# Kernel optimization log

Hardware: AMD Instinct MI355X
Metric: run time of the kernel (lower is better)

## Reference

```python
import jax, jax.numpy as jnp
import numpy as np

DIM = 1024
HEADS = 16
HDIM = DIM // HEADS
MLP_HID = 4096
LN_EPS = 1e-5
NORM_EPS = 1e-12  # F.normalize eps


def _layernorm(x, g, b):
    mu = jnp.mean(x, axis=-1, keepdims=True)
    var = jnp.mean(jnp.square(x - mu), axis=-1, keepdims=True)
    return (x - mu) / jnp.sqrt(var + LN_EPS) * g + b


def _l2norm(x):
    n = jnp.linalg.norm(x, axis=-1, keepdims=True)
    return x / jnp.maximum(n, NORM_EPS)


def setup_inputs() -> dict:
    key = jax.random.key(0)
    ks = jax.random.split(key, 8)
    s = 0.02
    x = jax.random.normal(ks[0], (2, 2048, DIM), dtype=jnp.float32)
    w_qkv = jax.random.normal(ks[1], (3 * DIM, DIM), dtype=jnp.float32) * s  # torch Linear weight (out,in)
    w_proj = jax.random.normal(ks[2], (DIM, DIM), dtype=jnp.float32) * s
    temp = jnp.ones((HEADS, 1, 1), dtype=jnp.float32)
    w1 = jax.random.normal(ks[3], (MLP_HID, DIM), dtype=jnp.float32) * s
    b1 = jnp.zeros((MLP_HID,), dtype=jnp.float32)
    w2 = jax.random.normal(ks[4], (DIM, MLP_HID), dtype=jnp.float32) * s
    b2 = jnp.zeros((DIM,), dtype=jnp.float32)
    ln1_g = jnp.ones((DIM,), dtype=jnp.float32)
    ln1_b = jnp.zeros((DIM,), dtype=jnp.float32)
    ln2_g = jnp.ones((DIM,), dtype=jnp.float32)
    ln2_b = jnp.zeros((DIM,), dtype=jnp.float32)
    return {"x": x, "ln1_g": ln1_g, "ln1_b": ln1_b, "w_qkv": w_qkv,
            "w_proj": w_proj, "temp": temp, "ln2_g": ln2_g, "ln2_b": ln2_b,
            "w1": w1, "b1": b1, "w2": w2, "b2": b2}


def reference(x, ln1_g, ln1_b, w_qkv, w_proj, temp, ln2_g, ln2_b, w1, b1, w2, b2):
    b, n, c = x.shape
    # --- MHSA with L2-normalized q,k and learnable per-head temperature ---
    h = _layernorm(x, ln1_g, ln1_b)
    qkv = h @ w_qkv.T                             # [b,n,3c]
    qkv = qkv.reshape(b, n, 3, HEADS, HDIM).transpose(2, 0, 3, 1, 4)  # [3,b,h,n,d]
    q, k, v = qkv[0], qkv[1], qkv[2]
    q = _l2norm(q)
    k = _l2norm(k)
    attn = jnp.einsum('bhnd,bhmd->bhnm', q, k) * temp  # temp [h,1,1] broadcasts
    attn = jax.nn.softmax(attn, axis=-1)
    out = jnp.einsum('bhnm,bhmd->bhnd', attn, v)       # [b,h,n,d]
    out = out.transpose(0, 2, 1, 3).reshape(b, n, c)
    x = x + out @ w_proj.T
    # --- MLP ---
    h = _layernorm(x, ln2_g, ln2_b)
    h = jax.nn.gelu(h @ w1.T + b1, approximate=False)
    x = x + h @ w2.T + b2
    return x
```

## Files before the change

kernel.cpp:

```cpp
#include <hip/hip_runtime.h>
#include <cstdint>
#include <cstddef>

typedef unsigned short u16;
typedef __attribute__((ext_vector_type(8))) short short8;
typedef __attribute__((ext_vector_type(4))) float f32x4;
typedef __attribute__((ext_vector_type(4))) float float4v;
typedef __attribute__((ext_vector_type(4))) u16 u16x4;

__device__ __forceinline__ u16 f2bf(float f) {
  union { float f; uint32_t u; } v; v.f = f;
  uint32_t u = v.u;
  return (u16)((u + 0x7FFFu + ((u >> 16) & 1u)) >> 16);
}
__device__ __forceinline__ float bf2f(u16 s) {
  union { uint32_t u; float f; } v; v.u = ((uint32_t)s) << 16; return v.f;
}

__device__ __forceinline__ float fast_exp2(float x) {
#if __has_builtin(__builtin_amdgcn_exp2f)
  return __builtin_amdgcn_exp2f(x);
#else
  return exp2f(x);
#endif
}

__device__ __forceinline__ void gload16(const u16* g, u16* l) {
  __builtin_amdgcn_global_load_lds((const __attribute__((address_space(1))) void*)g,
                                   (__attribute__((address_space(3))) void*)l,
                                   16, 0, 0);
}

__global__ __launch_bounds__(256) void k_cvt(const float* __restrict__ in, u16* __restrict__ out, int n4) {
  int i = blockIdx.x * 256 + threadIdx.x;
  if (i >= n4) return;
  float4v v = *(const float4v*)(in + (size_t)i * 4);
  u16x4 o;
  #pragma unroll
  for (int j = 0; j < 4; j++) o[j] = f2bf(v[j]);
  *(u16x4*)(out + (size_t)i * 4) = o;
}

__global__ __launch_bounds__(256) void k_ln(const float* __restrict__ x, const float* __restrict__ g,
                                            const float* __restrict__ b, u16* __restrict__ out) {
  int row = blockIdx.x, tid = threadIdx.x;
  int wid = tid >> 6;
  const float* xr = x + (size_t)row * 1024;
  float4v v = *(const float4v*)(xr + tid * 4);
  float s = v[0] + v[1] + v[2] + v[3];
  float sq = v[0]*v[0] + v[1]*v[1] + v[2]*v[2] + v[3]*v[3];
  #pragma unroll
  for (int m = 1; m <= 32; m <<= 1) { s += __shfl_xor(s, m); sq += __shfl_xor(sq, m); }
  __shared__ float ss[4], ssq[4];
  if ((tid & 63) == 0) { ss[wid] = s; ssq[wid] = sq; }
  __syncthreads();
  s = ss[0] + ss[1] + ss[2] + ss[3];
  sq = ssq[0] + ssq[1] + ssq[2] + ssq[3];
  float mu = s * (1.0f/1024.0f);
  float var = sq * (1.0f/1024.0f) - mu*mu;
  float rs = rsqrtf(var + 1e-5f);
  u16x4 o;
  #pragma unroll
  for (int j = 0; j < 4; j++) {
    float y = (v[j] - mu) * rs * g[tid*4+j] + b[tid*4+j];
    o[j] = f2bf(y);
  }
  *(u16x4*)(out + (size_t)row * 1024 + tid * 4) = o;
}

__global__ __launch_bounds__(256) void k_redln(const float* __restrict__ x, const u16* __restrict__ P,
                                               const float* __restrict__ g, const float* __restrict__ b,
                                               float* __restrict__ x1, u16* __restrict__ h2) {
  int row = blockIdx.x, tid = threadIdx.x;
  int wid = tid >> 6;
  size_t off = (size_t)row * 1024 + tid * 4;
  float4v v = *(const float4v*)(x + off);
  #pragma unroll
  for (int z = 0; z < 4; z++) {
    u16x4 p = *(const u16x4*)(P + (size_t)z * 4194304 + off);
    #pragma unroll
    for (int j = 0; j < 4; j++) v[j] += bf2f(p[j]);
  }
  *(float4v*)(x1 + off) = v;
  float s = v[0] + v[1] + v[2] + v[3];
  float sq = v[0]*v[0] + v[1]*v[1] + v[2]*v[2] + v[3]*v[3];
  #pragma unroll
  for (int m = 1; m <= 32; m <<= 1) { s += __shfl_xor(s, m); sq += __shfl_xor(sq, m); }
  __shared__ float ss[4], ssq[4];
  if ((tid & 63) == 0) { ss[wid] = s; ssq[wid] = sq; }
  __syncthreads();
  s = ss[0] + ss[1] + ss[2] + ss[3];
  sq = ssq[0] + ssq[1] + ssq[2] + ssq[3];
  float mu = s * (1.0f/1024.0f);
  float var = sq * (1.0f/1024.0f) - mu*mu;
  float rs = rsqrtf(var + 1e-5f);
  u16x4 o;
  #pragma unroll
  for (int j = 0; j < 4; j++) o[j] = f2bf((v[j] - mu) * rs * g[tid*4+j] + b[tid*4+j]);
  *(u16x4*)(h2 + off) = o;
}

template<int EPI>
__global__ __launch_bounds__(512, 2) void k_g256(const u16* __restrict__ A, const u16* __restrict__ B,
                                                 const float* __restrict__ bias, u16* __restrict__ Cb,
                                                 int M, int N, int K, int Ksub) {
  extern __shared__ __align__(16) u16 smem[];
  int tid = threadIdx.x;
  int gx = gridDim.x;
  int lin = blockIdx.y * gx + blockIdx.x;
  int nwg = gx * gridDim.y;
  int cpx = nwg >> 3;
  int swz = (lin & 7) * cpx + (lin >> 3);
  int bx = swz % gx, by = swz / gx;
  int m0 = by * 256, n0 = bx * 256;
  int kbase = blockIdx.z * Ksub;
  int wid = tid >> 6, lane = tid & 63;
  int wm = wid >> 2, wn = wid & 3;
  int l15 = lane & 15, l16 = lane >> 4;

  f32x4 acc[8][4] = {};
  int nt = Ksub >> 5;

  auto STAGE = [&](int bsel, int kb) {
    u16* abase = smem + bsel * 16384;
    u16* bbase = abase + 8192;
    #pragma unroll
    for (int i = 0; i < 2; i++) {
      int c = i*512 + tid;
      int R = c >> 3, p = c & 7;
      int sp = p ^ (R & 7);
      int r = 2*R + (sp >> 2);
      int g = sp & 3;
      gload16(A + (size_t)(m0 + r)*K + kb + g*8, abase + c*8);
      gload16(B + (size_t)(n0 + r)*K + kb + g*8, bbase + c*8);
    }
  };

  STAGE(0, kbase);
  STAGE(1, kbase + 32);

  for (int t = 0; t < nt; ++t) {
    if (t + 1 < nt) asm volatile("s_waitcnt vmcnt(4)" ::: "memory");
    else            asm volatile("s_waitcnt vmcnt(0)" ::: "memory");
    __builtin_amdgcn_sched_barrier(0);
    __builtin_amdgcn_s_barrier();
    __builtin_amdgcn_sched_barrier(0);
    if (t + 2 < nt) STAGE((t + 2) % 3, kbase + (t + 2) * 32);
    const u16* ab = smem + (t % 3) * 16384;
    const u16* bb = ab + 8192;
    short8 af[8], bf[4];
    #pragma unroll
    for (int mf = 0; mf < 8; mf++) {
      int r = wm*128 + mf*16 + l15;
      int R = r >> 1;
      int sp = ((r & 1)*4 + l16) ^ (R & 7);
      af[mf] = *(const short8*)(ab + R*64 + sp*8);
    }
    #pragma unroll
    for (int nf = 0; nf < 4; nf++) {
      int r = wn*64 + nf*16 + l15;
      int R = r >> 1;
      int sp = ((r & 1)*4 + l16) ^ (R & 7);
      bf[nf] = *(const short8*)(bb + R*64 + sp*8);
    }
    asm volatile("s_waitcnt lgkmcnt(0)" ::: "memory");
    __builtin_amdgcn_sched_barrier(0);
    __builtin_amdgcn_s_setprio(1);
    #pragma unroll
    for (int mf = 0; mf < 8; mf++)
      #pragma unroll
      for (int nf = 0; nf < 4; nf++)
        acc[mf][nf] = __builtin_amdgcn_mfma_f32_16x16x32_bf16(af[mf], bf[nf], acc[mf][nf], 0, 0, 0);
    __builtin_amdgcn_s_setprio(0);
  }

  size_t zoff = (EPI == 6) ? (size_t)blockIdx.z * M * N : 0;
  #pragma unroll
  for (int mf = 0; mf < 8; mf++) {
    #pragma unroll
    for (int nf = 0; nf < 4; nf++) {
      int col = n0 + wn*64 + nf*16 + l15;
      #pragma unroll
      for (int r = 0; r < 4; r++) {
        int row = m0 + wm*128 + mf*16 + l16*4 + r;
        float v = acc[mf][nf][r];
        if constexpr (EPI == 2) { v += bias[col]; v = 0.5f*v*(1.0f + erff(v*0.70710678118f)); }
        Cb[zoff + (size_t)row*N + col] = f2bf(v);
      }
    }
  }
}

template<int HASB>
__global__ __launch_bounds__(256) void k_red4(const float* __restrict__ base, const float* __restrict__ bias,
                                              const u16* __restrict__ P, float* __restrict__ out) {
  int i = blockIdx.x * 256 + threadIdx.x;
  float4v v = *(const float4v*)(base + (size_t)i * 4);
  if constexpr (HASB) {
    float4v bb = *(const float4v*)(bias + (size_t)(i & 255) * 4);
    #pragma unroll
    for (int j = 0; j < 4; j++) v[j] += bb[j];
  }
  #pragma unroll
  for (int z = 0; z < 4; z++) {
    u16x4 p = *(const u16x4*)(P + (size_t)z * 4194304 + (size_t)i * 4);
    #pragma unroll
    for (int j = 0; j < 4; j++) v[j] += bf2f(p[j]);
  }
  *(float4v*)(out + (size_t)i * 4) = v;
}

__global__ __launch_bounds__(256) void k_prep(const u16* __restrict__ qkv, const float* __restrict__ temp,
                                              u16* __restrict__ Qn, u16* __restrict__ Kn, u16* __restrict__ Vt) {
  int grp = blockIdx.x, bh = blockIdx.y;
  int b = bh >> 4, h = bh & 15;
  int tid = threadIdx.x, wid = tid >> 6, lane = tid & 63;
  int n0 = grp * 64;
  __shared__ __align__(16) u16 vs[64*64];
  float tmp = temp[h] * 1.44269504f;
  for (int j = 0; j < 16; j++) {
    int tl = wid + 4*j;
    size_t roff = (size_t)((b*2048) + n0 + tl) * 3072;
    float q = bf2f(qkv[roff + h*64 + lane]);
    float k = bf2f(qkv[roff + 1024 + h*64 + lane]);
    u16 vraw = qkv[roff + 2048 + h*64 + lane];
    float sq = q*q, sk = k*k;
    #pragma unroll
    for (int m = 1; m <= 32; m <<= 1) { sq += __shfl_xor(sq, m); sk += __shfl_xor(sk, m); }
    float qs = tmp / fmaxf(sqrtf(sq), 1e-12f);
    float ksc = 1.0f / fmaxf(sqrtf(sk), 1e-12f);
    size_t obase = ((size_t)bh*2048 + n0 + tl)*64 + lane;
    Qn[obase] = f2bf(q * qs);
    Kn[obase] = f2bf(k * ksc);
    vs[tl*64 + lane] = vraw;
  }
  __syncthreads();
  int d = tid & 63, chunk = tid >> 6;
  u16 vals[16];
  #pragma unroll
  for (int jj = 0; jj < 16; jj++) vals[jj] = vs[(chunk*16 + jj)*64 + d];
  short8 w0, w1v;
  #pragma unroll
  for (int j = 0; j < 8; j++) { w0[j] = (short)vals[j]; w1v[j] = (short)vals[8+j]; }
  size_t vo = ((size_t)bh*64 + d)*2048 + n0 + chunk*16;
  *(short8*)(Vt + vo) = w0;
  *(short8*)(Vt + vo + 8) = w1v;
}

__global__ __launch_bounds__(256) void k_attn(const u16* __restrict__ Qn, const u16* __restrict__ Kn,
                                              const u16* __restrict__ Vt, const float* __restrict__ temp,
                                              u16* __restrict__ Out) {
  __shared__ __align__(16) u16 Ks[2][64*64];
  __shared__ __align__(16) u16 Vs[2][64*64];
  __shared__ __align__(16) u16 Ps[4*2*16*64];
  int lin = blockIdx.y * gridDim.x + blockIdx.x;
  int c = lin & 7, t5 = lin >> 3;
  int bh = c*4 + (t5 >> 4);
  int qg = t5 & 15;
  int b = bh >> 4, h = bh & 15;
  int tid = threadIdx.x, wid = tid >> 6, lane = tid & 63;
  int l15 = lane & 15, l16 = lane >> 4;
  size_t base = (size_t)bh * 2048 * 64;
  size_t vbase = (size_t)bh * 64 * 2048;
  int q0 = qg*128 + wid*32;
  float m2 = fabsf(temp[h]) * 1.44269504f;
  short8 qf[2][2];
  #pragma unroll
  for (int g = 0; g < 2; g++)
    #pragma unroll
    for (int ks = 0; ks < 2; ks++)
      qf[g][ks] = *(const short8*)(Qn + base + (size_t)(q0 + g*16 + l15)*64 + ks*32 + l16*8);
  f32x4 o[2][4] = {};
  float lrow[2] = {0.f, 0.f};
  u16* Pw = Ps + wid*2048;
  uint32_t* Pw32 = (uint32_t*)Pw;

  auto STAGE = [&](int bsel, int kv0) {
    #pragma unroll
    for (int i = 0; i < 2; i++) {
      int base_row = wid*16 + i*8;
      int row = base_row + (lane >> 3);
      int gslot = (lane & 7) ^ (row & 7);
      gload16(Kn + base + (size_t)(kv0 + row)*64 + gslot*8, &Ks[bsel][base_row*64]);
      gload16(Vt + vbase + (size_t)row*2048 + kv0 + gslot*8, &Vs[bsel][base_row*64]);
    }
  };

  STAGE(0, 0);
  __syncthreads();
  int cur = 0;
  for (int kv0 = 0; kv0 < 2048; kv0 += 64) {
    if (kv0 + 64 < 2048) STAGE(cur ^ 1, kv0 + 64);
    f32x4 s[2][4] = {};
    #pragma unroll
    for (int ks = 0; ks < 2; ks++) {
      short8 kf[4];
      #pragma unroll
      for (int nt = 0; nt < 4; nt++) {
        int row = nt*16 + l15;
        kf[nt] = *(const short8*)&Ks[cur][row*64 + (((ks*4 + l16) ^ (row&7))*8)];
      }
      #pragma unroll
      for (int nt = 0; nt < 4; nt++) {
        s[0][nt] = __builtin_amdgcn_mfma_f32_16x16x32_bf16(kf[nt], qf[0][ks], s[0][nt], 0, 0, 0);
        s[1][nt] = __builtin_amdgcn_mfma_f32_16x16x32_bf16(kf[nt], qf[1][ks], s[1][nt], 0, 0, 0);
      }
    }
    #pragma unroll
    for (int g = 0; g < 2; g++) {
      float tsum = 0.f;
      #pragma unroll
      for (int nt = 0; nt < 4; nt++) {
        #pragma unroll
        for (int rp = 0; rp < 2; rp++) {
          float p0 = fast_exp2(s[g][nt][2*rp]   - m2);
          float p1 = fast_exp2(s[g][nt][2*rp+1] - m2);
          tsum += p0 + p1;
          uint32_t pk;
          asm("v_cvt_pk_bf16_f32 %0, %1, %2" : "=v"(pk) : "v"(p0), "v"(p1));
          int w = nt*8 + l16*2 + rp;
          int slot = w >> 2;
          Pw32[g*512 + l15*32 + ((slot ^ (l15 & 7))*4) + (w & 3)] = pk;
        }
      }
      lrow[g] += tsum;
    }
    asm volatile("s_waitcnt lgkmcnt(0)" ::: "memory");
    __builtin_amdgcn_sched_barrier(0);
    #pragma unroll
    for (int ks = 0; ks < 2; ks++) {
      short8 vf[4];
      #pragma unroll
      for (int dt = 0; dt < 4; dt++) {
        int row = dt*16 + l15;
        vf[dt] = *(const short8*)&Vs[cur][row*64 + (((ks*4 + l16) ^ (row&7))*8)];
      }
      short8 pf0 = *(const short8*)&Pw[0*1024 + l15*64 + (((ks*4 + l16) ^ (l15&7))*8)];
      short8 pf1 = *(const short8*)&Pw[1*1024 + l15*64 + (((ks*4 + l16) ^ (l15&7))*8)];
      #pragma unroll
      for (int dt = 0; dt < 4; dt++) {
        o[0][dt] = __builtin_amdgcn_mfma_f32_16x16x32_bf16(vf[dt], pf0, o[0][dt], 0, 0, 0);
        o[1][dt] = __builtin_amdgcn_mfma_f32_16x16x32_bf16(vf[dt], pf1, o[1][dt], 0, 0, 0);
      }
    }
    __syncthreads();
    cur ^= 1;
  }
  #pragma unroll
  for (int g = 0; g < 2; g++) {
    float l = lrow[g];
    l += __shfl_xor(l, 16);
    l += __shfl_xor(l, 32);
    float rl = 1.0f / l;
    int tok = b*2048 + q0 + g*16 + l15;
    #pragma unroll
    for (int dt = 0; dt < 4; dt++) {
      u16x4 ov;
      #pragma unroll
      for (int r = 0; r < 4; r++) ov[r] = f2bf(o[g][dt][r] * rl);
      *(u16x4*)(Out + (size_t)tok*1024 + h*64 + dt*16 + l16*4) = ov;
    }
  }
}

static constexpr size_t OFF_WQKV  = 0;
static constexpr size_t OFF_WPROJ = OFF_WQKV  + 6291456;
static constexpr size_t OFF_W1    = OFF_WPROJ + 2097152;
static constexpr size_t OFF_W2    = OFF_W1    + 8388608;
static constexpr size_t OFF_HBF   = OFF_W2    + 8388608;
static constexpr size_t OFF_H2BF  = OFF_HBF   + 8388608;
static constexpr size_t OFF_QKVBF = OFF_H2BF  + 8388608;
static constexpr size_t OFF_QN    = OFF_QKVBF + 25165824;
static constexpr size_t OFF_KN    = OFF_QN    + 8388608;
static constexpr size_t OFF_VT    = OFF_KN    + 8388608;
static constexpr size_t OFF_AOUT  = OFF_VT    + 8388608;
static constexpr size_t OFF_X1    = OFF_AOUT  + 8388608;
static constexpr size_t OFF_HID   = OFF_X1    + 16777216;

extern "C" void kernel_launch(void* const* d_in, const int* in_sizes, int n_in,
                              void* d_out, int out_size, void* d_ws, size_t ws_size,
                              hipStream_t stream) {
  (void)in_sizes; (void)n_in; (void)out_size; (void)ws_size;
  const float* x     = (const float*)d_in[0];
  const float* ln1g  = (const float*)d_in[1];
  const float* ln1b  = (const float*)d_in[2];
  const float* wqkv  = (const float*)d_in[3];
  const float* wproj = (const float*)d_in[4];
  const float* temp  = (const float*)d_in[5];
  const float* ln2g  = (const float*)d_in[6];
  const float* ln2b  = (const float*)d_in[7];
  const float* w1    = (const float*)d_in[8];
  const float* b1    = (const float*)d_in[9];
  const float* w2    = (const float*)d_in[10];
  const float* b2    = (const float*)d_in[11];

  char* ws = (char*)d_ws;
  u16* wqkv_bf  = (u16*)(ws + OFF_WQKV);
  u16* wproj_bf = (u16*)(ws + OFF_WPROJ);
  u16* w1_bf    = (u16*)(ws + OFF_W1);
  u16* w2_bf    = (u16*)(ws + OFF_W2);
  u16* h_bf     = (u16*)(ws + OFF_HBF);
  u16* h2_bf    = (u16*)(ws + OFF_H2BF);
  u16* qkv_bf   = (u16*)(ws + OFF_QKVBF);
  u16* Qn       = (u16*)(ws + OFF_QN);
  u16* Kn       = (u16*)(ws + OFF_KN);
  u16* Vt       = (u16*)(ws + OFF_VT);
  u16* aout_bf  = (u16*)(ws + OFF_AOUT);
  float* x1     = (float*)(ws + OFF_X1);
  u16* hid_bf   = (u16*)(ws + OFF_HID);
  u16* part_p   = (u16*)(ws + OFF_HID);
  u16* part_m   = (u16*)(ws + OFF_QN);
  float* outf   = (float*)d_out;

  static bool attr_done = false;
  if (!attr_done) {
    hipFuncSetAttribute((const void*)k_g256<2>, hipFuncAttributeMaxDynamicSharedMemorySize, 98304);
    hipFuncSetAttribute((const void*)k_g256<4>, hipFuncAttributeMaxDynamicSharedMemorySize, 98304);
    hipFuncSetAttribute((const void*)k_g256<6>, hipFuncAttributeMaxDynamicSharedMemorySize, 98304);
    attr_done = true;
  }

  k_cvt<<<3072, 256, 0, stream>>>(wqkv,  wqkv_bf,  786432);
  k_cvt<<<1024, 256, 0, stream>>>(wproj, wproj_bf, 262144);
  k_cvt<<<4096, 256, 0, stream>>>(w1,    w1_bf,    1048576);
  k_cvt<<<4096, 256, 0, stream>>>(w2,    w2_bf,    1048576);

  k_ln<<<4096, 256, 0, stream>>>(x, ln1g, ln1b, h_bf);
  k_g256<4><<<dim3(12, 16), 512, 98304, stream>>>(h_bf, wqkv_bf, nullptr, qkv_bf, 4096, 3072, 1024, 1024);
  k_prep<<<dim3(32, 32), 256, 0, stream>>>(qkv_bf, temp, Qn, Kn, Vt);
  k_attn<<<dim3(16, 32), 256, 0, stream>>>(Qn, Kn, Vt, temp, aout_bf);
  k_g256<6><<<dim3(4, 16, 4), 512, 98304, stream>>>(aout_bf, wproj_bf, nullptr, part_p, 4096, 1024, 1024, 256);
  k_redln<<<4096, 256, 0, stream>>>(x, part_p, ln2g, ln2b, x1, h2_bf);
  k_g256<2><<<dim3(16, 16), 512, 98304, stream>>>(h2_bf, w1_bf, b1, hid_bf, 4096, 4096, 1024, 1024);
  k_g256<6><<<dim3(4, 16, 4), 512, 98304, stream>>>(hid_bf, w2_bf, nullptr, part_m, 4096, 1024, 4096, 1024);
  k_red4<1><<<4096, 256, 0, stream>>>(x1, b2, part_m, outf);
}
```

Baseline: 260.8 us.

## Keep attention probabilities in registers by permuting K rows to match MFMA layout

Reorders which K rows each S-tile MFMA consumes so the accumulator layout of QK^T matches the B-operand layout needed for the PV MFMA. The softmax probabilities are packed directly into register fragments instead of going through a shared-memory P buffer, which removes the LDS writes, the lgkmcnt wait and the reads. The LDS swizzle key and the staging index mapping are changed to suit the new row access pattern. The risk is extra register pressure and a changed bank-conflict profile on K reads.

```diff
diff --git a/kernel.cpp b/kernel.cpp
--- a/kernel.cpp
+++ b/kernel.cpp
@@ -247,12 +247,13 @@
   *(short8*)(Vt + vo + 8) = w1v;
 }
 
+__device__ __forceinline__ int akey(int row) { return (row & 3) | (((row >> 3) & 1) << 2); }
+
 __global__ __launch_bounds__(256) void k_attn(const u16* __restrict__ Qn, const u16* __restrict__ Kn,
                                               const u16* __restrict__ Vt, const float* __restrict__ temp,
                                               u16* __restrict__ Out) {
   __shared__ __align__(16) u16 Ks[2][64*64];
   __shared__ __align__(16) u16 Vs[2][64*64];
-  __shared__ __align__(16) u16 Ps[4*2*16*64];
   int lin = blockIdx.y * gridDim.x + blockIdx.x;
   int c = lin & 7, t5 = lin >> 3;
   int bh = c*4 + (t5 >> 4);
@@ -272,17 +273,16 @@
       qf[g][ks] = *(const short8*)(Qn + base + (size_t)(q0 + g*16 + l15)*64 + ks*32 + l16*8);
   f32x4 o[2][4] = {};
   float lrow[2] = {0.f, 0.f};
-  u16* Pw = Ps + wid*2048;
-  uint32_t* Pw32 = (uint32_t*)Pw;
+  int prow = (l15 & 3) + 8*(l15 >> 2);
 
   auto STAGE = [&](int bsel, int kv0) {
     #pragma unroll
     for (int i = 0; i < 2; i++) {
-      int base_row = wid*16 + i*8;
-      int row = base_row + (lane >> 3);
-      int gslot = (lane & 7) ^ (row & 7);
-      gload16(Kn + base + (size_t)(kv0 + row)*64 + gslot*8, &Ks[bsel][base_row*64]);
-      gload16(Vt + vbase + (size_t)row*2048 + kv0 + gslot*8, &Vs[bsel][base_row*64]);
+      int cc = i*256 + tid;
+      int row = cc >> 3, p = cc & 7;
+      int g = p ^ akey(row);
+      gload16(Kn + base + (size_t)(kv0 + row)*64 + g*8, &Ks[bsel][(i*256 + wid*64)*8]);
+      gload16(Vt + vbase + (size_t)row*2048 + kv0 + g*8, &Vs[bsel][(i*256 + wid*64)*8]);
     }
   };
 
@@ -293,54 +293,52 @@
     if (kv0 + 64 < 2048) STAGE(cur ^ 1, kv0 + 64);
     f32x4 s[2][4] = {};
     #pragma unroll
-    for (int ks = 0; ks < 2; ks++) {
-      short8 kf[4];
-      #pragma unroll
-      for (int nt = 0; nt < 4; nt++) {
-        int row = nt*16 + l15;
-        kf[nt] = *(const short8*)&Ks[cur][row*64 + (((ks*4 + l16) ^ (row&7))*8)];
+    for (int dks = 0; dks < 2; dks++) {
+      #pragma unroll
+      for (int ss = 0; ss < 4; ss++) {
+        int row = (ss & 1)*4 + (ss >> 1)*32 + prow;
+        short8 kf = *(const short8*)&Ks[cur][row*64 + ((dks*4 + l16) ^ akey(row))*8];
+        s[0][ss] = __builtin_amdgcn_mfma_f32_16x16x32_bf16(kf, qf[0][dks], s[0][ss], 0, 0, 0);
+        s[1][ss] = __builtin_amdgcn_mfma_f32_16x16x32_bf16(kf, qf[1][dks], s[1][ss], 0, 0, 0);
       }
-      #pragma unroll
-      for (int nt = 0; nt < 4; nt++) {
-        s[0][nt] = __builtin_amdgcn_mfma_f32_16x16x32_bf16(kf[nt], qf[0][ks], s[0][nt], 0, 0, 0);
-        s[1][nt] = __builtin_amdgcn_mfma_f32_16x16x32_bf16(kf[nt], qf[1][ks], s[1][nt], 0, 0, 0);
-      }
-    }
+    }
+    short8 pf[2][2];
     #pragma unroll
     for (int g = 0; g < 2; g++) {
       float tsum = 0.f;
       #pragma unroll
-      for (int nt = 0; nt < 4; nt++) {
+      for (int kvs = 0; kvs < 2; kvs++) {
+        float e[8];
         #pragma unroll
-        for (int rp = 0; rp < 2; rp++) {
-          float p0 = fast_exp2(s[g][nt][2*rp]   - m2);
-          float p1 = fast_exp2(s[g][nt][2*rp+1] - m2);
-          tsum += p0 + p1;
+        for (int r = 0; r < 4; r++) {
+          e[r]   = fast_exp2(s[g][kvs*2][r]   - m2);
+          e[4+r] = fast_exp2(s[g][kvs*2+1][r] - m2);
+        }
+        #pragma unroll
+        for (int r = 0; r < 8; r++) tsum += e[r];
+        union { uint32_t u[4]; short8 v; } pu;
+        #pragma unroll
+        for (int w = 0; w < 4; w++) {
           uint32_t pk;
-          asm("v_cvt_pk_bf16_f32 %0, %1, %2" : "=v"(pk) : "v"(p0), "v"(p1));
-          int w = nt*8 + l16*2 + rp;
-          int slot = w >> 2;
-          Pw32[g*512 + l15*32 + ((slot ^ (l15 & 7))*4) + (w & 3)] = pk;
+          asm("v_cvt_pk_bf16_f32 %0, %1, %2" : "=v"(pk) : "v"(e[2*w]), "v"(e[2*w+1]));
+          pu.u[w] = pk;
         }
+        pf[g][kvs] = pu.v;
       }
       lrow[g] += tsum;
     }
-    asm volatile("s_waitcnt lgkmcnt(0)" ::: "memory");
-    __builtin_amdgcn_sched_barrier(0);
-    #pragma unroll
-    for (int ks = 0; ks < 2; ks++) {
+    #pragma unroll
+    for (int kvs = 0; kvs < 2; kvs++) {
       short8 vf[4];
       #pragma unroll
       for (int dt = 0; dt < 4; dt++) {
         int row = dt*16 + l15;
-        vf[dt] = *(const short8*)&Vs[cur][row*64 + (((ks*4 + l16) ^ (row&7))*8)];
+        vf[dt] = *(const short8*)&Vs[cur][row*64 + (((kvs*4 + l16) ^ akey(row))*8)];
       }
-      short8 pf0 = *(const short8*)&Pw[0*1024 + l15*64 + (((ks*4 + l16) ^ (l15&7))*8)];
-      short8 pf1 = *(const short8*)&Pw[1*1024 + l15*64 + (((ks*4 + l16) ^ (l15&7))*8)];
       #pragma unroll
       for (int dt = 0; dt < 4; dt++) {
-        o[0][dt] = __builtin_amdgcn_mfma_f32_16x16x32_bf16(vf[dt], pf0, o[0][dt], 0, 0, 0);
-        o[1][dt] = __builtin_amdgcn_mfma_f32_16x16x32_bf16(vf[dt], pf1, o[1][dt], 0, 0, 0);
+        o[0][dt] = __builtin_amdgcn_mfma_f32_16x16x32_bf16(vf[dt], pf[0][kvs], o[0][dt], 0, 0, 0);
+        o[1][dt] = __builtin_amdgcn_mfma_f32_16x16x32_bf16(vf[dt], pf[1][kvs], o[1][dt], 0, 0, 0);
       }
     }
     __syncthreads();
```

Measured after the change: 253.0 us. 1.03x faster.
